# Kernel tuning notes

Measured on AMD Instinct MI355X. Metric: run time of the kernel, lower is better.

Reference implementation:

```python
import jax, jax.numpy as jnp
import numpy as np

N, E, D, R = 100000, 640000, 128, 4


def setup_inputs() -> dict:
    key = jax.random.key(0)
    ks = jax.random.split(key, 5)
    x = jax.random.normal(ks[0], (N, D), dtype=jnp.float32)
    edge_index = jax.random.randint(ks[1], (2, E), 0, N, dtype=jnp.int64)
    edge_attr = jax.random.randint(ks[2], (E,), 0, R, dtype=jnp.int64)
    # Per-relation GraphConv weights (conv_layer instantiated as PyG GraphConv, aggr='add')
    W_rel = jax.random.normal(ks[3], (R, D, D), dtype=jnp.float32) / np.sqrt(D).astype(np.float32)
    b_rel = jnp.zeros((R, D), dtype=jnp.float32)
    W_root = jax.random.normal(ks[4], (R, D, D), dtype=jnp.float32) / np.sqrt(D).astype(np.float32)
    b_root = jnp.zeros((R, D), dtype=jnp.float32)
    return {"x": x, "edge_index": edge_index, "edge_attr": edge_attr,
            "W_rel": W_rel, "b_rel": b_rel, "W_root": W_root, "b_root": b_root}


def reference(x, edge_index, edge_attr, W_rel, b_rel, W_root, b_root):
    # Fused equivalent of: sum_r tanh(GraphConv_r(x, edge_index[:, edge_attr==r]))
    # GraphConv_r(x, ei) = segment_sum(x[src], dst) @ W_rel[r] + b_rel[r] + x @ W_root[r] + b_root[r]
    src, dst = edge_index[0], edge_index[1]
    msgs = x[src]                                  # [E, D] single gather for all relations
    seg = dst * R + edge_attr                      # combined (node, relation) segment id
    agg = jax.ops.segment_sum(msgs, seg, num_segments=N * R).reshape(N, R, D)
    rel = jnp.einsum('nrd,rde->nre', agg, W_rel) + b_rel    # [N, R, D]
    root = jnp.einsum('nd,rde->nre', x, W_root) + b_root    # [N, R, D]
    return jnp.tanh(rel + root).sum(axis=1)       # accumulate over relations -> [N, D]
```

## Files before the change

### kernel.cpp

```cpp
#include <hip/hip_runtime.h>
#include <stdint.h>

#define D 128
#define RNUM 4
#define TM 32
#define CAP 16
#define LSTRIDE 272

typedef unsigned short u16;
typedef __attribute__((ext_vector_type(8))) short short8;
typedef __attribute__((ext_vector_type(4))) float floatx4;

__device__ inline u16 f2bf(float f) {
  union { float f; uint32_t u; } c; c.f = f;
  uint32_t r = (c.u + 0x7FFFu + ((c.u >> 16) & 1u)) >> 16;
  return (u16)r;
}
__device__ inline uint32_t pack2(float a, float b) {
  return (uint32_t)f2bf(a) | ((uint32_t)f2bf(b) << 16);
}
__device__ inline float bflo(uint32_t w) {
  union { uint32_t u; float f; } c; c.u = w << 16; return c.f;
}
__device__ inline float bfhi(uint32_t w) {
  union { uint32_t u; float f; } c; c.u = w & 0xFFFF0000u; return c.f;
}

__device__ inline float fast_tanh(float v) {
  float a = fabsf(v);
  float e = __builtin_amdgcn_exp2f(a * 2.8853900817779268f);
  float t = 1.0f - 2.0f * __builtin_amdgcn_rcpf(e + 1.0f);
  return copysignf(t, v);
}

__global__ void prep_kernel(const float* __restrict__ x,
                            const float* __restrict__ W_rel, const float* __restrict__ b_rel,
                            const float* __restrict__ W_root, const float* __restrict__ b_root,
                            u16* __restrict__ Wt, float* __restrict__ bias,
                            u16* __restrict__ x16, uint32_t* __restrict__ cursor,
                            int total8, int nseg) {
  int idx = blockIdx.x * 256 + threadIdx.x;
  if (idx < total8) {
    const float4* s = (const float4*)(x + (size_t)idx * 8);
    float4 lo = s[0], hi = s[1];
    uint4 pk;
    pk.x = pack2(lo.x, lo.y); pk.y = pack2(lo.z, lo.w);
    pk.z = pack2(hi.x, hi.y); pk.w = pack2(hi.z, hi.w);
    *(uint4*)(x16 + (size_t)idx * 8) = pk;
  }
  if (idx < nseg) cursor[idx] = 0u;
  if (idx < RNUM * D) bias[idx] = b_rel[idx] + b_root[idx];
  if (idx < RNUM * D * 2 * D) {
    int k   = idx & 255;
    int col = (idx >> 8) & 127;
    int r   = idx >> 15;
    float v = (k < D) ? W_rel[((size_t)r * D + k) * D + col]
                      : W_root[((size_t)r * D + (k - D)) * D + col];
    Wt[idx] = f2bf(v);
  }
}

__global__ void bin_kernel(const int* __restrict__ ei, const int* __restrict__ ea,
                           uint32_t* __restrict__ cursor, uint32_t* __restrict__ bins, int E) {
  int t = blockIdx.x * 256 + threadIdx.x;
  if (t >= E) return;
  uint32_t seg = (uint32_t)ei[E + t] * 4u + (uint32_t)ea[t];
  uint32_t pos = atomicAdd(&cursor[seg], 1u);
  if (pos < (uint32_t)CAP) bins[(size_t)seg * CAP + pos] = (uint32_t)ei[t];
}

__global__ __launch_bounds__(512, 6) void fused_kernel(
    const u16* __restrict__ x16, const uint32_t* __restrict__ bins,
    const uint32_t* __restrict__ cursor,
    const u16* __restrict__ Wt, const float* __restrict__ bias,
    float* __restrict__ out, int N) {
  __shared__ __align__(16) u16 sA[5 * TM * D];
  __shared__ __align__(16) uint32_t sList[8 * LSTRIDE];

  const int tid = threadIdx.x;
  const int w = tid >> 6, l = tid & 63;
  const int nodeBase = blockIdx.x * TM;

  {
    uint4 z4 = {0u, 0u, 0u, 0u};
    uint4* za = (uint4*)sA;
#pragma unroll
    for (int i = 0; i < 4; ++i) za[tid + i * 512] = z4;
    uint4* zl = (uint4*)sList;
    for (int i = tid; i < 8 * LSTRIDE / 4; i += 512) zl[i] = z4;
  }

  {
    int c = tid & 15, node = tid >> 4;
    int gnode = nodeBase + node;
    uint4 pk = {0u, 0u, 0u, 0u};
    if (gnode < N) pk = *(const uint4*)(x16 + (size_t)gnode * D + c * 8);
    *(uint4*)&sA[4 * (TM * D) + node * D + ((c ^ (node & 7)) << 3)] = pk;
  }
  __syncthreads();

  {
    const uint32_t segBase = (uint32_t)blockIdx.x * (TM * RNUM) + (uint32_t)w * 16;
    uint32_t cnt = 0;
    if (l < 16) {
      uint32_t c = cursor[segBase + l];
      cnt = c < (uint32_t)CAP ? c : (uint32_t)CAP;
    }
    uint32_t run = cnt;
#pragma unroll
    for (int dlt = 1; dlt < 16; dlt <<= 1) {
      int v = __shfl_up((int)run, dlt, 16);
      if ((l & 15) >= dlt) run += (uint32_t)v;
    }
    uint32_t offx = run - cnt;
    uint32_t total = (uint32_t)__builtin_amdgcn_readfirstlane(__shfl((int)run, 15));

    uint32_t* wl = &sList[w * LSTRIDE];
    {
      int row = l >> 2, sb = (l & 3) * 4;
      uint32_t rowcnt = (uint32_t)__shfl((int)cnt, row);
      uint32_t rowoff = (uint32_t)__shfl((int)offx, row);
      uint4 rc4 = *(const uint4*)(bins + (size_t)(segBase + row) * CAP + sb);
      uint32_t tag = (uint32_t)row << 20;
      if ((uint32_t)(sb + 0) < rowcnt) wl[rowoff + sb + 0] = (rc4.x & 0x1FFFFu) | tag;
      if ((uint32_t)(sb + 1) < rowcnt) wl[rowoff + sb + 1] = (rc4.y & 0x1FFFFu) | tag;
      if ((uint32_t)(sb + 2) < rowcnt) wl[rowoff + sb + 2] = (rc4.z & 0x1FFFFu) | tag;
      if ((uint32_t)(sb + 3) < rowcnt) wl[rowoff + sb + 3] = (rc4.w & 0x1FFFFu) | tag;
    }
    __asm volatile("s_waitcnt lgkmcnt(0)");

    const int ch = l >> 2, q2 = (l & 3) * 2;
    int curRow = -1;
    float ax = 0.f, ay = 0.f;
    for (uint32_t i = 0; i < total; i += 8) {
      uint4 ra = *(const uint4*)&wl[i];
      uint4 rb = *(const uint4*)&wl[i + 4];
      uint32_t r8[8] = {ra.x, ra.y, ra.z, ra.w, rb.x, rb.y, rb.z, rb.w};
      uint32_t wv[8];
#pragma unroll
      for (int j = 0; j < 8; ++j)
        wv[j] = *(const uint32_t*)(x16 + (size_t)(r8[j] & 0x1FFFFu) * D + 2 * l);
#pragma unroll
      for (int j = 0; j < 8; ++j) {
        if (i + (uint32_t)j < total) {
          int rj = (int)(r8[j] >> 20);
          if (rj != curRow) {
            if (curRow >= 0) {
              int node_ = w * 4 + (curRow >> 2), rel_ = curRow & 3;
              int idx_ = rel_ * (TM * D) + node_ * D + ((ch ^ (node_ & 7)) << 3) + q2;
              *(uint32_t*)&sA[idx_] = pack2(ax, ay);
            }
            ax = 0.f; ay = 0.f; curRow = rj;
          }
          ax += bflo(wv[j]); ay += bfhi(wv[j]);
        }
      }
    }
    if (curRow >= 0) {
      int node_ = w * 4 + (curRow >> 2), rel_ = curRow & 3;
      int idx_ = rel_ * (TM * D) + node_ * D + ((ch ^ (node_ & 7)) << 3) + q2;
      *(uint32_t*)&sA[idx_] = pack2(ax, ay);
    }
  }
  __syncthreads();

  const int lrow = l & 15, lhi = l >> 4;
  floatx4 oacc[2];
  oacc[0] = (floatx4){0.f, 0.f, 0.f, 0.f};
  oacc[1] = (floatx4){0.f, 0.f, 0.f, 0.f};

  for (int r = 0; r < RNUM; ++r) {
    floatx4 acc[2];
    acc[0] = (floatx4){0.f, 0.f, 0.f, 0.f};
    acc[1] = (floatx4){0.f, 0.f, 0.f, 0.f};

#pragma unroll
    for (int ks = 0; ks < 8; ++ks) {
      const u16* Abase = (ks < 4) ? (sA + r * (TM * D)) : (sA + 4 * (TM * D));
      const int cRead = (ks & 3) * 4 + lhi;
      short8 afr[2];
#pragma unroll
      for (int m = 0; m < 2; ++m) {
        int node = m * 16 + lrow;
        afr[m] = *(const short8*)&Abase[node * D + ((cRead ^ (node & 7)) << 3)];
      }
      int col = w * 16 + lrow;
      short8 bfr = *(const short8*)(Wt + ((size_t)(r * D + col) * (2 * D) + ks * 32 + lhi * 8));
#pragma unroll
      for (int m = 0; m < 2; ++m)
        acc[m] = __builtin_amdgcn_mfma_f32_16x16x32_bf16(afr[m], bfr, acc[m], 0, 0, 0);
    }

    float bb = bias[r * D + w * 16 + lrow];
#pragma unroll
    for (int m = 0; m < 2; ++m)
#pragma unroll
      for (int j = 0; j < 4; ++j)
        oacc[m][j] += fast_tanh(acc[m][j] + bb);
  }

#pragma unroll
  for (int m = 0; m < 2; ++m) {
#pragma unroll
    for (int j = 0; j < 4; ++j) {
      int node = nodeBase + m * 16 + lhi * 4 + j;
      if (node < N) out[(size_t)node * D + w * 16 + lrow] = oacc[m][j];
    }
  }
}

extern "C" void kernel_launch(void* const* d_in, const int* in_sizes, int n_in,
                              void* d_out, int out_size, void* d_ws, size_t ws_size,
                              hipStream_t stream) {
  const float* x      = (const float*)d_in[0];
  const int*   ei     = (const int*)d_in[1];
  const int*   ea     = (const int*)d_in[2];
  const float* W_rel  = (const float*)d_in[3];
  const float* b_rel  = (const float*)d_in[4];
  const float* W_root = (const float*)d_in[5];
  const float* b_root = (const float*)d_in[6];
  float* out = (float*)d_out;

  const int N = in_sizes[0] / D;
  const int E = in_sizes[2];
  const int NB = (N + TM - 1) / TM;
  const int NSEG = N * RNUM;
  const int total8 = N * (D / 8);

  size_t o = 0;
  auto nxt = [&](size_t bytes) { size_t p = o; o += (bytes + 255) & ~(size_t)255; return p; };
  u16*      Wt     = (u16*)((char*)d_ws + nxt((size_t)RNUM * D * 2 * D * 2));
  float*    bias   = (float*)((char*)d_ws + nxt((size_t)RNUM * D * 4));
  uint32_t* cursor = (uint32_t*)((char*)d_ws + nxt((size_t)NSEG * 4));
  uint32_t* bins   = (uint32_t*)((char*)d_ws + nxt((size_t)NSEG * CAP * 4));
  u16*      x16    = (u16*)((char*)d_ws + nxt((size_t)N * D * 2));

  prep_kernel<<<(total8 + 255) / 256, 256, 0, stream>>>(x, W_rel, b_rel, W_root, b_root,
                                                        Wt, bias, x16, cursor, total8, NSEG);
  bin_kernel<<<(E + 255) / 256, 256, 0, stream>>>(ei, ea, cursor, bins, E);
  fused_kernel<<<NB, 512, 0, stream>>>(x16, bins, cursor, Wt, bias, out, N);
}
```

Baseline: 168.4 us.

## Split fused gather+GEMM kernel into separate gather and GEMM kernels

Splits the fused kernel in two. A new gather kernel sums neighbor features per (node, relation) segment and writes the bf16 aggregates to a global buffer. A GEMM kernel then loads the aggregates and x into LDS and runs the MFMA/tanh reduction. The aim is to decouple the latency-bound gather from the GEMM so each runs at a better occupancy, at the cost of an extra round trip of about 100 MB of aggregates through global memory and one more launch.

```diff
diff --git a/kernel.cpp b/kernel.cpp
--- a/kernel.cpp
+++ b/kernel.cpp
@@ -69,98 +69,114 @@
   if (pos < (uint32_t)CAP) bins[(size_t)seg * CAP + pos] = (uint32_t)ei[t];
 }
 
-__global__ __launch_bounds__(512, 6) void fused_kernel(
+__global__ __launch_bounds__(256, 8) void gather_kernel(
     const u16* __restrict__ x16, const uint32_t* __restrict__ bins,
-    const uint32_t* __restrict__ cursor,
+    const uint32_t* __restrict__ cursor, u16* __restrict__ agg16, int nseg) {
+  __shared__ __align__(16) uint32_t sList[4 * LSTRIDE];
+
+  const int tid = threadIdx.x;
+  const int w = tid >> 6, l = tid & 63;
+  const uint32_t segBase = (uint32_t)blockIdx.x * 64 + (uint32_t)w * 16;
+
+  {
+    uint4 z4 = {0u, 0u, 0u, 0u};
+    uint4* zl = (uint4*)sList;
+#pragma unroll
+    for (int i = 0; i < 2; ++i) {
+      int idx = tid + i * 256;
+      if (idx < 4 * LSTRIDE / 4) zl[idx] = z4;
+    }
+  }
+  __syncthreads();
+
+  uint32_t cnt = 0;
+  if (l < 16 && segBase + l < (uint32_t)nseg) {
+    uint32_t c = cursor[segBase + l];
+    cnt = c < (uint32_t)CAP ? c : (uint32_t)CAP;
+  }
+  uint32_t run = cnt;
+#pragma unroll
+  for (int dlt = 1; dlt < 16; dlt <<= 1) {
+    int v = __shfl_up((int)run, dlt, 16);
+    if ((l & 15) >= dlt) run += (uint32_t)v;
+  }
+  uint32_t offx = run - cnt;
+  uint32_t total = (uint32_t)__builtin_amdgcn_readfirstlane(__shfl((int)run, 15));
+
+  uint32_t* wl = &sList[w * LSTRIDE];
+  {
+    int row = l >> 2, sb = (l & 3) * 4;
+    uint32_t rowcnt = (uint32_t)__shfl((int)cnt, row);
+    uint32_t rowoff = (uint32_t)__shfl((int)offx, row);
+    uint4 rc4 = *(const uint4*)(bins + (size_t)(segBase + row) * CAP + sb);
+    uint32_t tag = (uint32_t)row << 20;
+    if ((uint32_t)(sb + 0) < rowcnt) wl[rowoff + sb + 0] = (rc4.x & 0x1FFFFu) | tag;
+    if ((uint32_t)(sb + 1) < rowcnt) wl[rowoff + sb + 1] = (rc4.y & 0x1FFFFu) | tag;
+    if ((uint32_t)(sb + 2) < rowcnt) wl[rowoff + sb + 2] = (rc4.z & 0x1FFFFu) | tag;
+    if ((uint32_t)(sb + 3) < rowcnt) wl[rowoff + sb + 3] = (rc4.w & 0x1FFFFu) | tag;
+  }
+  __asm volatile("s_waitcnt lgkmcnt(0)");
+
+  int curRow = -1;
+  uint32_t written = 0;
+  float ax = 0.f, ay = 0.f;
+  for (uint32_t i = 0; i < total; i += 8) {
+    uint4 ra = *(const uint4*)&wl[i];
+    uint4 rb = *(const uint4*)&wl[i + 4];
+    uint32_t r8[8] = {ra.x, ra.y, ra.z, ra.w, rb.x, rb.y, rb.z, rb.w};
+    uint32_t wv[8];
+#pragma unroll
+    for (int j = 0; j < 8; ++j)
+      wv[j] = *(const uint32_t*)(x16 + (size_t)(r8[j] & 0x1FFFFu) * D + 2 * l);
+#pragma unroll
+    for (int j = 0; j < 8; ++j) {
+      if (i + (uint32_t)j < total) {
+        int rj = (int)(r8[j] >> 20);
+        if (rj != curRow) {
+          if (curRow >= 0) {
+            *(uint32_t*)(agg16 + (size_t)(segBase + curRow) * D + 2 * l) = pack2(ax, ay);
+            written |= 1u << curRow;
+          }
+          ax = 0.f; ay = 0.f; curRow = rj;
+        }
+        ax += bflo(wv[j]); ay += bfhi(wv[j]);
+      }
+    }
+  }
+  if (curRow >= 0) {
+    *(uint32_t*)(agg16 + (size_t)(segBase + curRow) * D + 2 * l) = pack2(ax, ay);
+    written |= 1u << curRow;
+  }
+  for (int t = 0; t < 16; ++t) {
+    if (!(written & (1u << t)) && segBase + t < (uint32_t)nseg)
+      *(uint32_t*)(agg16 + (size_t)(segBase + t) * D + 2 * l) = 0u;
+  }
+}
+
+__global__ __launch_bounds__(512, 6) void gemm_kernel(
+    const u16* __restrict__ agg16, const u16* __restrict__ x16,
     const u16* __restrict__ Wt, const float* __restrict__ bias,
     float* __restrict__ out, int N) {
   __shared__ __align__(16) u16 sA[5 * TM * D];
-  __shared__ __align__(16) uint32_t sList[8 * LSTRIDE];
 
   const int tid = threadIdx.x;
   const int w = tid >> 6, l = tid & 63;
   const int nodeBase = blockIdx.x * TM;
 
-  {
-    uint4 z4 = {0u, 0u, 0u, 0u};
-    uint4* za = (uint4*)sA;
-#pragma unroll
-    for (int i = 0; i < 4; ++i) za[tid + i * 512] = z4;
-    uint4* zl = (uint4*)sList;
-    for (int i = tid; i < 8 * LSTRIDE / 4; i += 512) zl[i] = z4;
-  }
-
-  {
-    int c = tid & 15, node = tid >> 4;
+#pragma unroll
+  for (int k = 0; k < 5; ++k) {
+    int id = tid + k * 512;
+    int slot = id >> 9;
+    int within = id & 511;
+    int c = within & 15, node = within >> 4;
     int gnode = nodeBase + node;
     uint4 pk = {0u, 0u, 0u, 0u};
-    if (gnode < N) pk = *(const uint4*)(x16 + (size_t)gnode * D + c * 8);
-    *(uint4*)&sA[4 * (TM * D) + node * D + ((c ^ (node & 7)) << 3)] = pk;
-  }
-  __syncthreads();
-
-  {
-    const uint32_t segBase = (uint32_t)blockIdx.x * (TM * RNUM) + (uint32_t)w * 16;
-    uint32_t cnt = 0;
-    if (l < 16) {
-      uint32_t c = cursor[segBase + l];
-      cnt = c < (uint32_t)CAP ? c : (uint32_t)CAP;
-    }
-    uint32_t run = cnt;
-#pragma unroll
-    for (int dlt = 1; dlt < 16; dlt <<= 1) {
-      int v = __shfl_up((int)run, dlt, 16);
-      if ((l & 15) >= dlt) run += (uint32_t)v;
-    }
-    uint32_t offx = run - cnt;
-    uint32_t total = (uint32_t)__builtin_amdgcn_readfirstlane(__shfl((int)run, 15));
-
-    uint32_t* wl = &sList[w * LSTRIDE];
-    {
-      int row = l >> 2, sb = (l & 3) * 4;
-      uint32_t rowcnt = (uint32_t)__shfl((int)cnt, row);
-      uint32_t rowoff = (uint32_t)__shfl((int)offx, row);
-      uint4 rc4 = *(const uint4*)(bins + (size_t)(segBase + row) * CAP + sb);
-      uint32_t tag = (uint32_t)row << 20;
-      if ((uint32_t)(sb + 0) < rowcnt) wl[rowoff + sb + 0] = (rc4.x & 0x1FFFFu) | tag;
-      if ((uint32_t)(sb + 1) < rowcnt) wl[rowoff + sb + 1] = (rc4.y & 0x1FFFFu) | tag;
-      if ((uint32_t)(sb + 2) < rowcnt) wl[rowoff + sb + 2] = (rc4.z & 0x1FFFFu) | tag;
-      if ((uint32_t)(sb + 3) < rowcnt) wl[rowoff + sb + 3] = (rc4.w & 0x1FFFFu) | tag;
-    }
-    __asm volatile("s_waitcnt lgkmcnt(0)");
-
-    const int ch = l >> 2, q2 = (l & 3) * 2;
-    int curRow = -1;
-    float ax = 0.f, ay = 0.f;
-    for (uint32_t i = 0; i < total; i += 8) {
-      uint4 ra = *(const uint4*)&wl[i];
-      uint4 rb = *(const uint4*)&wl[i + 4];
-      uint32_t r8[8] = {ra.x, ra.y, ra.z, ra.w, rb.x, rb.y, rb.z, rb.w};
-      uint32_t wv[8];
-#pragma unroll
-      for (int j = 0; j < 8; ++j)
-        wv[j] = *(const uint32_t*)(x16 + (size_t)(r8[j] & 0x1FFFFu) * D + 2 * l);
-#pragma unroll
-      for (int j = 0; j < 8; ++j) {
-        if (i + (uint32_t)j < total) {
-          int rj = (int)(r8[j] >> 20);
-          if (rj != curRow) {
-            if (curRow >= 0) {
-              int node_ = w * 4 + (curRow >> 2), rel_ = curRow & 3;
-              int idx_ = rel_ * (TM * D) + node_ * D + ((ch ^ (node_ & 7)) << 3) + q2;
-              *(uint32_t*)&sA[idx_] = pack2(ax, ay);
-            }
-            ax = 0.f; ay = 0.f; curRow = rj;
-          }
-          ax += bflo(wv[j]); ay += bfhi(wv[j]);
-        }
-      }
-    }
-    if (curRow >= 0) {
-      int node_ = w * 4 + (curRow >> 2), rel_ = curRow & 3;
-      int idx_ = rel_ * (TM * D) + node_ * D + ((ch ^ (node_ & 7)) << 3) + q2;
-      *(uint32_t*)&sA[idx_] = pack2(ax, ay);
-    }
+    if (gnode < N) {
+      const u16* src = (slot < 4) ? (agg16 + ((size_t)gnode * 4 + slot) * D + c * 8)
+                                  : (x16 + (size_t)gnode * D + c * 8);
+      pk = *(const uint4*)src;
+    }
+    *(uint4*)&sA[slot * (TM * D) + node * D + ((c ^ (node & 7)) << 3)] = pk;
   }
   __syncthreads();
 
@@ -226,6 +242,7 @@
   const int NB = (N + TM - 1) / TM;
   const int NSEG = N * RNUM;
   const int total8 = N * (D / 8);
+  const int GB = (NSEG + 63) / 64;
 
   size_t o = 0;
   auto nxt = [&](size_t bytes) { size_t p = o; o += (bytes + 255) & ~(size_t)255; return p; };
@@ -234,9 +251,11 @@
   uint32_t* cursor = (uint32_t*)((char*)d_ws + nxt((size_t)NSEG * 4));
   uint32_t* bins   = (uint32_t*)((char*)d_ws + nxt((size_t)NSEG * CAP * 4));
   u16*      x16    = (u16*)((char*)d_ws + nxt((size_t)N * D * 2));
+  u16*      agg16  = (u16*)((char*)d_ws + nxt((size_t)NSEG * D * 2));
 
   prep_kernel<<<(total8 + 255) / 256, 256, 0, stream>>>(x, W_rel, b_rel, W_root, b_root,
                                                         Wt, bias, x16, cursor, total8, NSEG);
   bin_kernel<<<(E + 255) / 256, 256, 0, stream>>>(ei, ea, cursor, bins, E);
-  fused_kernel<<<NB, 512, 0, stream>>>(x16, bins, cursor, Wt, bias, out, N);
-}
+  gather_kernel<<<GB, 256, 0, stream>>>(x16, bins, cursor, agg16, NSEG);
+  gemm_kernel<<<NB, 512, 0, stream>>>(agg16, x16, Wt, bias, out, N);
+}
```

Result: slower. 204.9 us (+21.6%).
